# Performance work log

Measured on AMD Instinct MI355X. Metric: run time of the kernel, lower is better.

The kernel has to match this reference:

```python
import jax, jax.numpy as jnp
import numpy as np

B, T, C = 16, 2048, 128
HEAD_SIZE = 128

def setup_inputs() -> dict:
    key = jax.random.key(0)
    k1, k2, k3, k4 = jax.random.split(key, 4)
    x = jax.random.normal(k1, (B, T, C), dtype=jnp.float32)
    # nn.Linear(N_EMBED, head_size, bias=False) weight shape: [head_size, N_EMBED]
    scale = (1.0 / np.sqrt(C)).astype(np.float32)
    Wq = jax.random.normal(k2, (HEAD_SIZE, C), dtype=jnp.float32) * scale
    Wk = jax.random.normal(k3, (HEAD_SIZE, C), dtype=jnp.float32) * scale
    Wv = jax.random.normal(k4, (HEAD_SIZE, C), dtype=jnp.float32) * scale
    return {"x": x, "Wq": Wq, "Wk": Wk, "Wv": Wv}

def reference(x, Wq, Wk, Wv):
    Bd, Td, Cd = x.shape
    q = jnp.einsum('btc,hc->bth', x, Wq)  # [B,T,H]
    k = jnp.einsum('btc,hc->bth', x, Wk)
    v = jnp.einsum('btc,hc->bth', x, Wv)
    # NOTE: original scales by C**-0.5 (embedding dim), not head_size**-0.5
    scores = jnp.einsum('bth,bsh->bts', q, k) * (Cd ** -0.5)  # [B,T,T]
    causal = jnp.tril(jnp.ones((Td, Td), dtype=bool))
    scores = jnp.where(causal, scores, -jnp.inf)
    attn = jax.nn.softmax(scores, axis=-1)
    out = jnp.einsum('bts,bsh->bth', attn, v)  # [B,T,H]
    return out
```

## Files before the change

### kernel.cpp

```cpp
#include <hip/hip_runtime.h>
#include <hip/hip_bf16.h>

#define BB 16
#define TT 2048
#define CC 128
#define HH 128
#define NQT128 16

typedef __bf16 bf16x8 __attribute__((ext_vector_type(8)));
typedef float  f32x4  __attribute__((ext_vector_type(4)));

#define BTH       ((size_t)BB * TT * HH)
#define WBF_OFF   (3 * BTH)
#define PARTIAL_OFF_BYTES (3 * BTH * 2 + 3 * 128 * 128 * 2)
#define SLOT_BYTES 33280
#define SLOT_L_OFF 32768

static __device__ __forceinline__ bf16x8 load_cvt8(const float* p) {
    float4 a = *(const float4*)p;
    float4 b = *(const float4*)(p + 4);
    bf16x8 r;
    r[0] = (__bf16)a.x; r[1] = (__bf16)a.y; r[2] = (__bf16)a.z; r[3] = (__bf16)a.w;
    r[4] = (__bf16)b.x; r[5] = (__bf16)b.y; r[6] = (__bf16)b.z; r[7] = (__bf16)b.w;
    return r;
}

static __device__ __forceinline__ void load_lds16(const void* g, void* l) {
    __builtin_amdgcn_global_load_lds(
        (const __attribute__((address_space(1))) unsigned int*)g,
        (__attribute__((address_space(3))) unsigned int*)l, 16, 0, 0);
}

#define BAR_VM()   asm volatile("s_waitcnt vmcnt(0)\n\ts_barrier" ::: "memory")
#define BAR_LGKM() asm volatile("s_waitcnt lgkmcnt(0)\n\ts_barrier" ::: "memory")

__global__ __launch_bounds__(256) void wcvt_kernel(
    const float* __restrict__ Wq, const float* __restrict__ Wk,
    const float* __restrict__ Wv, __bf16* __restrict__ wbf)
{
    int idx = blockIdx.x * 256 + threadIdx.x;
    int which = idx >> 11;
    int rem = idx & 2047;
    int blk = rem >> 8;
    int r2  = rem & 255;
    int ks   = r2 >> 6;
    int lane = r2 & 63;
    int quad = lane >> 4, l16 = lane & 15;
    const float* src = (which == 0) ? Wq : (which == 1) ? Wk : Wv;
    float sc = (which == 0) ? (0.08838834764831845f * 1.4426950408889634f) : 1.0f;
    const float* p = src + (size_t)(blk * 16 + l16) * CC + ks * 32 + quad * 8;
    bf16x8 v;
    #pragma unroll
    for (int j = 0; j < 8; ++j) v[j] = (__bf16)(p[j] * sc);
    *(bf16x8*)(wbf + (size_t)which * 16384 + (((size_t)(blk * 4 + ks)) << 9) + lane * 8) = v;
}

#define TR_QK 132
#define TR_V  68

__global__ __launch_bounds__(256) void proj_kernel(
    const float* __restrict__ x, __bf16* __restrict__ ws)
{
    __shared__ float  xs[64 * 132];
    __shared__ __bf16 tr[128 * TR_V];

    const int lane = threadIdx.x & 63;
    const int wave = threadIdx.x >> 6;
    const int quad = lane >> 4;
    const int l16  = lane & 15;
    const int tid  = threadIdx.x;
    const int m0 = blockIdx.x * 64;
    const int b  = m0 / TT;
    const int t0 = m0 % TT;

    const __bf16* Wbf = ws + WBF_OFF;
    __bf16* Qs = ws;
    __bf16* Ks = ws + BTH;
    __bf16* Vs = ws + 2 * BTH;

    const float* xg = x + (size_t)m0 * CC;
    #pragma unroll
    for (int t = 0; t < 8; ++t) {
        int f = t * 256 + tid;
        int row = f >> 5, c4 = f & 31;
        float4 v = *(const float4*)(xg + (size_t)f * 4);
        *(float4*)(&xs[row * 132 + c4 * 4]) = v;
    }
    __syncthreads();

    bf16x8 xf[4];
    #pragma unroll
    for (int ks = 0; ks < 4; ++ks)
        xf[ks] = load_cvt8(&xs[(wave * 16 + l16) * 132 + ks * 32 + quad * 8]);

    #pragma unroll
    for (int which = 0; which < 2; ++which) {
        const __bf16* Wb = Wbf + (size_t)which * 16384;
        __bf16* dst = which ? Ks : Qs;
        #pragma unroll
        for (int nt = 0; nt < 8; ++nt) {
            f32x4 acc = {0.f, 0.f, 0.f, 0.f};
            #pragma unroll
            for (int ks = 0; ks < 4; ++ks) {
                bf16x8 wf = *(const bf16x8*)(Wb + (((size_t)(nt * 4 + ks)) << 9) + lane * 8);
                acc = __builtin_amdgcn_mfma_f32_16x16x32_bf16(xf[ks], wf, acc, 0, 0, 0);
            }
            #pragma unroll
            for (int r = 0; r < 4; ++r)
                tr[(wave * 16 + quad * 4 + r) * TR_QK + nt * 16 + l16] = (__bf16)acc[r];
        }
        asm volatile("s_waitcnt lgkmcnt(0)" ::: "memory");
        #pragma unroll
        for (int ks = 0; ks < 4; ++ks) {
            const __bf16* p = &tr[(wave * 16 + l16) * TR_QK + ks * 32 + quad * 8];
            uint2 lo = *(const uint2*)p;
            uint2 hi = *(const uint2*)(p + 4);
            uint4 v; v.x = lo.x; v.y = lo.y; v.z = hi.x; v.w = hi.y;
            __bf16* o = dst + (((size_t)(b * 128 + t0 / 16 + wave) * 4 + ks) << 9) + lane * 8;
            *(uint4*)o = v;
        }
        asm volatile("s_waitcnt lgkmcnt(0)" ::: "memory");
    }

    __syncthreads();
    const __bf16* Wv = Wbf + 2 * 16384;
    #pragma unroll
    for (int msub = 0; msub < 8; ++msub) {
        f32x4 acc = {0.f, 0.f, 0.f, 0.f};
        #pragma unroll
        for (int ks = 0; ks < 4; ++ks) {
            bf16x8 wf = *(const bf16x8*)(Wv + (((size_t)(msub * 4 + ks)) << 9) + lane * 8);
            acc = __builtin_amdgcn_mfma_f32_16x16x32_bf16(wf, xf[ks], acc, 0, 0, 0);
        }
        #pragma unroll
        for (int r = 0; r < 4; ++r)
            tr[(msub * 16 + quad * 4 + r) * TR_V + wave * 16 + l16] = (__bf16)acc[r];
    }
    __syncthreads();
    #pragma unroll
    for (int i = 0; i < 4; ++i) {
        int t32 = i >> 1;
        int h16 = wave * 2 + (i & 1);
        const __bf16* p = &tr[(h16 * 16 + l16) * TR_V + t32 * 32 + quad * 8];
        uint2 lo = *(const uint2*)p;
        uint2 hi = *(const uint2*)(p + 4);
        uint4 v; v.x = lo.x; v.y = lo.y; v.z = hi.x; v.w = hi.y;
        __bf16* o = Vs + (((size_t)(b * 64 + t0 / 32 + t32) * 8 + h16) << 9) + lane * 8;
        *(uint4*)o = v;
    }
}

#define S32 40
#define EXP_BIAS 16.0f

__global__ __launch_bounds__(256) void attn_kernel(
    const __bf16* __restrict__ ws, char* __restrict__ po,
    float* __restrict__ outp, int G, int SPB, int direct)
{
    __shared__ __bf16 ldsK[2][4096];
    __shared__ __bf16 ldsV[2][4096];
    __shared__ __bf16 lds_p[4 * 32 * S32];

    const int lane = threadIdx.x & 63;
    const int wave = threadIdx.x >> 6;
    const int quad = lane >> 4;
    const int l16  = lane & 15;
    const int lane8 = lane * 8;

    const int lin = blockIdx.x;
    const int b  = (lin & 7) * 2 + ((lin >> 3) & 1);
    const int s  = SPB - 1 - (lin >> 4);

    int acc = 0, qt = 0, seg = 0;
    for (int q = 0; q < NQT128; ++q) {
        int c = (2 * (q + 1) + G - 1) / G;
        if (s < acc + c) { qt = q; seg = s - acc; break; }
        acc += c;
    }
    const int kt0 = seg * G;
    int kt1 = 2 * (qt + 1);
    if (kt0 + G < kt1) kt1 = kt0 + G;
    const int segs_qt = (2 * (qt + 1) + G - 1) / G;
    const int dwrite = direct | (segs_qt == 1);

    const int tt0 = kt0 * 2, tt1 = kt1 * 2;
    const int qw = qt * 128 + wave * 32;
    int ttw = (qw + 63) >> 5;
    if (ttw > tt1) ttw = tt1;

    const __bf16* Qs = ws;
    const __bf16* Ks = ws + BTH;
    const __bf16* Vs = ws + 2 * BTH;

    bf16x8 qf[2][4];
    #pragma unroll
    for (int m = 0; m < 2; ++m)
        #pragma unroll
        for (int ks = 0; ks < 4; ++ks)
            qf[m][ks] = *(const bf16x8*)(Qs + (((size_t)(b * 128 + qt * 8 + wave * 2 + m) * 4 + ks) << 9) + lane8);

    float l_r[2][4];
    f32x4 o[2][8];
    #pragma unroll
    for (int m = 0; m < 2; ++m) {
        #pragma unroll
        for (int r = 0; r < 4; ++r) l_r[m][r] = 0.f;
        #pragma unroll
        for (int h8 = 0; h8 < 8; ++h8) o[m][h8] = (f32x4){0.f, 0.f, 0.f, 0.f};
    }

    __bf16* myP = lds_p + wave * 32 * S32;

    #define STAGE32(TTv, BUF)                                                       \
        do {                                                                        \
            const char* kb_ = (const char*)(Ks + (((size_t)(b * 128 + (TTv) * 2) * 4) << 9)); \
            const char* vb_ = (const char*)(Vs + (((size_t)(b * 64 + (TTv)) * 8) << 9));      \
            _Pragma("unroll")                                                       \
            for (int i_ = 0; i_ < 2; ++i_) {                                        \
                int c_ = wave * 2 + i_;                                             \
                load_lds16(kb_ + c_ * 1024 + (size_t)lane * 16, (char*)ldsK[BUF] + c_ * 1024); \
                load_lds16(vb_ + c_ * 1024 + (size_t)lane * 16, (char*)ldsV[BUF] + c_ * 1024); \
            }                                                                       \
        } while (0)

    STAGE32(tt0, 0);

    for (int tt = tt0; tt < tt1; ++tt) {
        const int cur = (tt - tt0) & 1;
        BAR_VM();
        if (tt + 1 < tt1) STAGE32(tt + 1, cur ^ 1);

        if (tt < ttw) {
            const char* lk = (const char*)ldsK[cur];
            const char* lv = (const char*)ldsV[cur];

            f32x4 s2[2][2];
            #pragma unroll
            for (int nsub = 0; nsub < 2; ++nsub) {
                bf16x8 kfr[4];
                #pragma unroll
                for (int ks = 0; ks < 4; ++ks)
                    kfr[ks] = *(const bf16x8*)(lk + ((nsub * 4 + ks) << 10) + lane * 16);
                #pragma unroll
                for (int m = 0; m < 2; ++m) {
                    f32x4 a2 = {0.f, 0.f, 0.f, 0.f};
                    #pragma unroll
                    for (int ks = 0; ks < 4; ++ks)
                        a2 = __builtin_amdgcn_mfma_f32_16x16x32_bf16(qf[m][ks], kfr[ks], a2, 0, 0, 0);
                    s2[m][nsub] = a2;
                }
            }

            const int k0 = tt * 32;
            #pragma unroll
            for (int m = 0; m < 2; ++m) {
                const int qr0m = qw + m * 16;
                if (k0 + 31 > qr0m) {
                    #pragma unroll
                    for (int nsub = 0; nsub < 2; ++nsub) {
                        int key = k0 + nsub * 16 + l16;
                        #pragma unroll
                        for (int r = 0; r < 4; ++r) {
                            int rowq = qr0m + quad * 4 + r;
                            if (key > rowq) s2[m][nsub][r] = -3e38f;
                        }
                    }
                }
                #pragma unroll
                for (int nsub = 0; nsub < 2; ++nsub) {
                    #pragma unroll
                    for (int r = 0; r < 4; ++r) {
                        float p = __builtin_amdgcn_exp2f(s2[m][nsub][r] - EXP_BIAS);
                        l_r[m][r] += p;
                        myP[(m * 16 + quad * 4 + r) * S32 + nsub * 16 + l16] = (__bf16)p;
                    }
                }
            }
            asm volatile("s_waitcnt lgkmcnt(0)" ::: "memory");

            bf16x8 pf[2];
            #pragma unroll
            for (int m = 0; m < 2; ++m)
                pf[m] = *(const bf16x8*)((const char*)myP + (size_t)(m * 16 + l16) * (S32 * 2) + quad * 16);

            #pragma unroll
            for (int h8 = 0; h8 < 8; ++h8) {
                bf16x8 v0 = *(const bf16x8*)(lv + (h8 << 10) + lane * 16);
                #pragma unroll
                for (int m = 0; m < 2; ++m)
                    o[m][h8] = __builtin_amdgcn_mfma_f32_16x16x32_bf16(pf[m], v0, o[m][h8], 0, 0, 0);
            }
        }
        BAR_LGKM();
    }

    #pragma unroll
    for (int m = 0; m < 2; ++m)
        #pragma unroll
        for (int r = 0; r < 4; ++r)
            #pragma unroll
            for (int j = 1; j <= 8; j <<= 1)
                l_r[m][r] += __shfl_xor(l_r[m][r], j, 64);

    if (dwrite) {
        #pragma unroll
        for (int m = 0; m < 2; ++m) {
            float inv[4];
            #pragma unroll
            for (int r = 0; r < 4; ++r) inv[r] = 1.0f / l_r[m][r];
            #pragma unroll
            for (int h8 = 0; h8 < 8; ++h8)
                #pragma unroll
                for (int r = 0; r < 4; ++r)
                    outp[(size_t)(b * TT + qw + m * 16 + quad * 4 + r) * HH + h8 * 16 + l16] = o[m][h8][r] * inv[r];
        }
    } else {
        char* slot = po + (size_t)(b * SPB + s) * SLOT_BYTES;
        __bf16* slot_o = (__bf16*)slot;
        float*  slot_l = (float*)(slot + SLOT_L_OFF);
        #pragma unroll
        for (int m = 0; m < 2; ++m) {
            #pragma unroll
            for (int h8 = 0; h8 < 8; ++h8)
                #pragma unroll
                for (int r = 0; r < 4; ++r)
                    slot_o[(size_t)(wave * 32 + m * 16 + quad * 4 + r) * 128 + h8 * 16 + l16] = (__bf16)o[m][h8][r];
            if (l16 == 0) {
                #pragma unroll
                for (int r = 0; r < 4; ++r)
                    slot_l[wave * 32 + m * 16 + quad * 4 + r] = l_r[m][r];
            }
        }
    }
}

__global__ __launch_bounds__(256) void reduce_kernel(
    const char* __restrict__ po, float* __restrict__ outp, int G, int SPB)
{
    __shared__ float lsum[32];
    const int qt  = blockIdx.x >> 2;
    const int qtr = blockIdx.x & 3;
    const int b   = blockIdx.y;
    const int tid = threadIdx.x;

    const int segs = (2 * (qt + 1) + G - 1) / G;
    if (segs == 1) return;

    int acc = 0;
    for (int qq = 0; qq < qt; ++qq) acc += (2 * (qq + 1) + G - 1) / G;
    const char* base = po + (size_t)(b * SPB + acc) * SLOT_BYTES;
    const int r0 = qtr * 32;

    if (tid < 32) {
        float v = 0.f;
        for (int sg = 0; sg < segs; ++sg)
            v += ((const float*)(base + (size_t)sg * SLOT_BYTES + SLOT_L_OFF))[r0 + tid];
        lsum[tid] = v;
    }
    __syncthreads();

    const int rsub = tid >> 4;
    const int cg   = tid & 15;
    float a[2][8];
    #pragma unroll
    for (int p = 0; p < 2; ++p)
        #pragma unroll
        for (int j = 0; j < 8; ++j) a[p][j] = 0.f;

    for (int sg = 0; sg < segs; ++sg) {
        const char* sb = base + (size_t)sg * SLOT_BYTES;
        #pragma unroll
        for (int p = 0; p < 2; ++p) {
            int row = r0 + rsub + p * 16;
            union { uint4 u; __bf16 h[8]; } v;
            v.u = *(const uint4*)(sb + ((size_t)row * 128 + cg * 8) * 2);
            #pragma unroll
            for (int j = 0; j < 8; ++j) a[p][j] += (float)v.h[j];
        }
    }

    #pragma unroll
    for (int p = 0; p < 2; ++p) {
        int row = r0 + rsub + p * 16;
        float inv = 1.0f / lsum[rsub + p * 16];
        float* op = outp + (size_t)(b * TT + qt * 128 + row) * HH + cg * 8;
        float4 o0 = {a[p][0] * inv, a[p][1] * inv, a[p][2] * inv, a[p][3] * inv};
        float4 o1 = {a[p][4] * inv, a[p][5] * inv, a[p][6] * inv, a[p][7] * inv};
        *(float4*)op = o0;
        *(float4*)(op + 4) = o1;
    }
}

extern "C" void kernel_launch(void* const* d_in, const int* in_sizes, int n_in,
                              void* d_out, int out_size, void* d_ws, size_t ws_size,
                              hipStream_t stream)
{
    const float* x  = (const float*)d_in[0];
    const float* Wq = (const float*)d_in[1];
    const float* Wk = (const float*)d_in[2];
    const float* Wv = (const float*)d_in[3];
    __bf16* ws = (__bf16*)d_ws;
    float* out = (float*)d_out;
    char* po   = (char*)d_ws + PARTIAL_OFF_BYTES;

    int G = 0, SPB = 0, direct = 1;
    const int cand[3] = {6, 8, 16};
    for (int ci = 0; ci < 3; ++ci) {
        int g = cand[ci], spb = 0;
        for (int q = 0; q < NQT128; ++q) spb += (2 * (q + 1) + g - 1) / g;
        size_t need = PARTIAL_OFF_BYTES + (size_t)spb * BB * SLOT_BYTES;
        if (need <= ws_size) { G = g; SPB = spb; direct = 0; break; }
    }
    if (direct) { G = 2 * NQT128; SPB = NQT128; }

    wcvt_kernel<<<24, 256, 0, stream>>>(Wq, Wk, Wv, ws + WBF_OFF);
    proj_kernel<<<512, 256, 0, stream>>>(x, ws);
    attn_kernel<<<SPB * 16, 256, 0, stream>>>(ws, po, out, G, SPB, direct);
    if (!direct) {
        dim3 rgrid(NQT128 * 4, BB);
        reduce_kernel<<<rgrid, 256, 0, stream>>>(po, out, G, SPB);
    }
}
```

Baseline: 135.4 us.

## Transpose QK MFMA, swizzle P in LDS, partial vmcnt waits, finer split

The attention inner loop swaps the MFMA operands so each lane holds one query row's scores. P can then be written as packed bf16x4 stores into an XOR-swizzled LDS buffer, and the row sum collapses to a two-step shuffle. The loop is unrolled by two so the next K/V tile is prefetched with a partial vmcnt(4) wait instead of a full drain before the barrier. V fragments are loaded up front, the exp bias is dropped, occupancy is hinted with launch_bounds(256,4), and split granularity 5 is added as the first candidate, which adds more partial slots and reduce work. Dropping the exp bias risks overflow if scores grow large.

```diff
diff --git a/kernel.cpp b/kernel.cpp
--- a/kernel.cpp
+++ b/kernel.cpp
@@ -8,6 +8,7 @@
 #define NQT128 16
 
 typedef __bf16 bf16x8 __attribute__((ext_vector_type(8)));
+typedef __bf16 bf16x4 __attribute__((ext_vector_type(4)));
 typedef float  f32x4  __attribute__((ext_vector_type(4)));
 
 #define BTH       ((size_t)BB * TT * HH)
@@ -31,7 +32,6 @@
         (__attribute__((address_space(3))) unsigned int*)l, 16, 0, 0);
 }
 
-#define BAR_VM()   asm volatile("s_waitcnt vmcnt(0)\n\ts_barrier" ::: "memory")
 #define BAR_LGKM() asm volatile("s_waitcnt lgkmcnt(0)\n\ts_barrier" ::: "memory")
 
 __global__ __launch_bounds__(256) void wcvt_kernel(
@@ -150,22 +150,20 @@
     }
 }
 
-#define S32 40
-#define EXP_BIAS 16.0f
-
-__global__ __launch_bounds__(256) void attn_kernel(
+__global__ __launch_bounds__(256, 4) void attn_kernel(
     const __bf16* __restrict__ ws, char* __restrict__ po,
     float* __restrict__ outp, int G, int SPB, int direct)
 {
     __shared__ __bf16 ldsK[2][4096];
     __shared__ __bf16 ldsV[2][4096];
-    __shared__ __bf16 lds_p[4 * 32 * S32];
+    __shared__ __bf16 lds_p[4096];
 
     const int lane = threadIdx.x & 63;
     const int wave = threadIdx.x >> 6;
     const int quad = lane >> 4;
     const int l16  = lane & 15;
     const int lane8 = lane * 8;
+    const int lo16 = lane * 16;
 
     const int lin = blockIdx.x;
     const int b  = (lin & 7) * 2 + ((lin >> 3) & 1);
@@ -199,115 +197,134 @@
         for (int ks = 0; ks < 4; ++ks)
             qf[m][ks] = *(const bf16x8*)(Qs + (((size_t)(b * 128 + qt * 8 + wave * 2 + m) * 4 + ks) << 9) + lane8);
 
-    float l_r[2][4];
+    float l_r[2] = {0.f, 0.f};
     f32x4 o[2][8];
     #pragma unroll
-    for (int m = 0; m < 2; ++m) {
-        #pragma unroll
-        for (int r = 0; r < 4; ++r) l_r[m][r] = 0.f;
+    for (int m = 0; m < 2; ++m)
         #pragma unroll
         for (int h8 = 0; h8 < 8; ++h8) o[m][h8] = (f32x4){0.f, 0.f, 0.f, 0.f};
-    }
-
-    __bf16* myP = lds_p + wave * 32 * S32;
-
-    #define STAGE32(TTv, BUF)                                                       \
-        do {                                                                        \
-            const char* kb_ = (const char*)(Ks + (((size_t)(b * 128 + (TTv) * 2) * 4) << 9)); \
-            const char* vb_ = (const char*)(Vs + (((size_t)(b * 64 + (TTv)) * 8) << 9));      \
-            _Pragma("unroll")                                                       \
-            for (int i_ = 0; i_ < 2; ++i_) {                                        \
-                int c_ = wave * 2 + i_;                                             \
-                load_lds16(kb_ + c_ * 1024 + (size_t)lane * 16, (char*)ldsK[BUF] + c_ * 1024); \
-                load_lds16(vb_ + c_ * 1024 + (size_t)lane * 16, (char*)ldsV[BUF] + c_ * 1024); \
-            }                                                                       \
+
+    char* myP = (char*)lds_p + wave * 2048;
+
+    const char* kg = (const char*)Ks + (size_t)b * 524288 + wave * 2048 + lo16;
+    const char* vg = (const char*)Vs + (size_t)b * 524288 + wave * 2048 + lo16;
+    char* const dKa[2] = {(char*)ldsK[0] + wave * 2048, (char*)ldsK[1] + wave * 2048};
+    char* const dVa[2] = {(char*)ldsV[0] + wave * 2048, (char*)ldsV[1] + wave * 2048};
+
+    #define STAGE(TTv, KD, VD)                                  \
+        do {                                                    \
+            size_t o_ = (size_t)(TTv) << 13;                    \
+            load_lds16(kg + o_,        (KD));                   \
+            load_lds16(kg + o_ + 1024, (KD) + 1024);            \
+            load_lds16(vg + o_,        (VD));                   \
+            load_lds16(vg + o_ + 1024, (VD) + 1024);            \
         } while (0)
 
-    STAGE32(tt0, 0);
-
-    for (int tt = tt0; tt < tt1; ++tt) {
-        const int cur = (tt - tt0) & 1;
-        BAR_VM();
-        if (tt + 1 < tt1) STAGE32(tt + 1, cur ^ 1);
-
-        if (tt < ttw) {
-            const char* lk = (const char*)ldsK[cur];
-            const char* lv = (const char*)ldsV[cur];
-
-            f32x4 s2[2][2];
-            #pragma unroll
-            for (int nsub = 0; nsub < 2; ++nsub) {
-                bf16x8 kfr[4];
-                #pragma unroll
-                for (int ks = 0; ks < 4; ++ks)
-                    kfr[ks] = *(const bf16x8*)(lk + ((nsub * 4 + ks) << 10) + lane * 16);
-                #pragma unroll
-                for (int m = 0; m < 2; ++m) {
-                    f32x4 a2 = {0.f, 0.f, 0.f, 0.f};
+    STAGE(tt0, dKa[0], dVa[0]);
+
+    for (int tp = tt0; tp < tt1; tp += 2) {
+        #pragma unroll
+        for (int hh = 0; hh < 2; ++hh) {
+            const int tt = tp + hh;
+            if (tt + 1 < tt1) {
+                STAGE(tt + 1, dKa[hh ^ 1], dVa[hh ^ 1]);
+                asm volatile("s_waitcnt vmcnt(4)" ::: "memory");
+            } else {
+                asm volatile("s_waitcnt vmcnt(0)" ::: "memory");
+            }
+            __builtin_amdgcn_s_barrier();
+
+            if (tt < ttw) {
+                const char* lk = (const char*)ldsK[hh];
+                const char* lv = (const char*)ldsV[hh];
+
+                f32x4 s2[2][2];
+                #pragma unroll
+                for (int nsub = 0; nsub < 2; ++nsub) {
+                    bf16x8 kfr[4];
                     #pragma unroll
                     for (int ks = 0; ks < 4; ++ks)
-                        a2 = __builtin_amdgcn_mfma_f32_16x16x32_bf16(qf[m][ks], kfr[ks], a2, 0, 0, 0);
-                    s2[m][nsub] = a2;
+                        kfr[ks] = *(const bf16x8*)(lk + ((nsub * 4 + ks) << 10) + lo16);
+                    #pragma unroll
+                    for (int m = 0; m < 2; ++m) {
+                        f32x4 a2 = {0.f, 0.f, 0.f, 0.f};
+                        #pragma unroll
+                        for (int ks = 0; ks < 4; ++ks)
+                            a2 = __builtin_amdgcn_mfma_f32_16x16x32_bf16(kfr[ks], qf[m][ks], a2, 0, 0, 0);
+                        s2[m][nsub] = a2;
+                    }
                 }
-            }
-
-            const int k0 = tt * 32;
-            #pragma unroll
-            for (int m = 0; m < 2; ++m) {
-                const int qr0m = qw + m * 16;
-                if (k0 + 31 > qr0m) {
-                    #pragma unroll
-                    for (int nsub = 0; nsub < 2; ++nsub) {
-                        int key = k0 + nsub * 16 + l16;
+
+                bf16x8 vr[8];
+                #pragma unroll
+                for (int h8 = 0; h8 < 8; ++h8)
+                    vr[h8] = *(const bf16x8*)(lv + (h8 << 10) + lo16);
+
+                const int k0 = tt * 32;
+                #pragma unroll
+                for (int m = 0; m < 2; ++m) {
+                    const int qrow = qw + m * 16 + l16;
+                    char* rowp = myP + m * 1024 + l16 * 64;
+                    const int swz = (l16 & 3) << 4;
+                    if (k0 + 31 > qw + m * 16) {
                         #pragma unroll
-                        for (int r = 0; r < 4; ++r) {
-                            int rowq = qr0m + quad * 4 + r;
-                            if (key > rowq) s2[m][nsub][r] = -3e38f;
+                        for (int nsub = 0; nsub < 2; ++nsub) {
+                            const int kb = k0 + nsub * 16 + quad * 4;
+                            bf16x4 pw;
+                            #pragma unroll
+                            for (int r = 0; r < 4; ++r) {
+                                float sv = (kb + r > qrow) ? -3e38f : s2[m][nsub][r];
+                                float p = __builtin_amdgcn_exp2f(sv);
+                                l_r[m] += p;
+                                pw[r] = (__bf16)p;
+                            }
+                            *(bf16x4*)(rowp + ((nsub * 32 + quad * 8) ^ swz)) = pw;
+                        }
+                    } else {
+                        #pragma unroll
+                        for (int nsub = 0; nsub < 2; ++nsub) {
+                            bf16x4 pw;
+                            #pragma unroll
+                            for (int r = 0; r < 4; ++r) {
+                                float p = __builtin_amdgcn_exp2f(s2[m][nsub][r]);
+                                l_r[m] += p;
+                                pw[r] = (__bf16)p;
+                            }
+                            *(bf16x4*)(rowp + ((nsub * 32 + quad * 8) ^ swz)) = pw;
                         }
                     }
                 }
-                #pragma unroll
-                for (int nsub = 0; nsub < 2; ++nsub) {
+                asm volatile("s_waitcnt lgkmcnt(0)" ::: "memory");
+
+                bf16x8 pf[2];
+                #pragma unroll
+                for (int m = 0; m < 2; ++m)
+                    pf[m] = *(const bf16x8*)(myP + m * 1024 + l16 * 64 + ((quad * 16) ^ ((l16 & 3) << 4)));
+
+                #pragma unroll
+                for (int h8 = 0; h8 < 8; ++h8)
                     #pragma unroll
-                    for (int r = 0; r < 4; ++r) {
-                        float p = __builtin_amdgcn_exp2f(s2[m][nsub][r] - EXP_BIAS);
-                        l_r[m][r] += p;
-                        myP[(m * 16 + quad * 4 + r) * S32 + nsub * 16 + l16] = (__bf16)p;
-                    }
-                }
+                    for (int m = 0; m < 2; ++m)
+                        o[m][h8] = __builtin_amdgcn_mfma_f32_16x16x32_bf16(pf[m], vr[h8], o[m][h8], 0, 0, 0);
             }
-            asm volatile("s_waitcnt lgkmcnt(0)" ::: "memory");
-
-            bf16x8 pf[2];
-            #pragma unroll
-            for (int m = 0; m < 2; ++m)
-                pf[m] = *(const bf16x8*)((const char*)myP + (size_t)(m * 16 + l16) * (S32 * 2) + quad * 16);
-
-            #pragma unroll
-            for (int h8 = 0; h8 < 8; ++h8) {
-                bf16x8 v0 = *(const bf16x8*)(lv + (h8 << 10) + lane * 16);
-                #pragma unroll
-                for (int m = 0; m < 2; ++m)
-                    o[m][h8] = __builtin_amdgcn_mfma_f32_16x16x32_bf16(pf[m], v0, o[m][h8], 0, 0, 0);
-            }
-        }
-        BAR_LGKM();
-    }
-
-    #pragma unroll
-    for (int m = 0; m < 2; ++m)
-        #pragma unroll
-        for (int r = 0; r < 4; ++r)
-            #pragma unroll
-            for (int j = 1; j <= 8; j <<= 1)
-                l_r[m][r] += __shfl_xor(l_r[m][r], j, 64);
+            BAR_LGKM();
+        }
+    }
+    #undef STAGE
+
+    #pragma unroll
+    for (int m = 0; m < 2; ++m) {
+        l_r[m] += __shfl_xor(l_r[m], 16, 64);
+        l_r[m] += __shfl_xor(l_r[m], 32, 64);
+    }
 
     if (dwrite) {
         #pragma unroll
         for (int m = 0; m < 2; ++m) {
             float inv[4];
             #pragma unroll
-            for (int r = 0; r < 4; ++r) inv[r] = 1.0f / l_r[m][r];
+            for (int r = 0; r < 4; ++r)
+                inv[r] = 1.0f / __shfl(l_r[m], (lane & 48) | (quad * 4 + r), 64);
             #pragma unroll
             for (int h8 = 0; h8 < 8; ++h8)
                 #pragma unroll
@@ -325,11 +342,8 @@
                 #pragma unroll
                 for (int r = 0; r < 4; ++r)
                     slot_o[(size_t)(wave * 32 + m * 16 + quad * 4 + r) * 128 + h8 * 16 + l16] = (__bf16)o[m][h8][r];
-            if (l16 == 0) {
-                #pragma unroll
-                for (int r = 0; r < 4; ++r)
-                    slot_l[wave * 32 + m * 16 + quad * 4 + r] = l_r[m][r];
-            }
+            if (quad == 0)
+                slot_l[wave * 32 + m * 16 + l16] = l_r[m];
         }
     }
 }
@@ -404,8 +418,8 @@
     char* po   = (char*)d_ws + PARTIAL_OFF_BYTES;
 
     int G = 0, SPB = 0, direct = 1;
-    const int cand[3] = {6, 8, 16};
-    for (int ci = 0; ci < 3; ++ci) {
+    const int cand[4] = {5, 6, 8, 16};
+    for (int ci = 0; ci < 4; ++ci) {
         int g = cand[ci], spb = 0;
         for (int q = 0; q < NQT128; ++q) spb += (2 * (q + 1) + g - 1) / g;
         size_t need = PARTIAL_OFF_BYTES + (size_t)spb * BB * SLOT_BYTES;
```

Result: slower. 193.0 us (+42.5%).
